# Kernel tuning notes

Hardware: AMD Instinct MI355X
Metric: run time of the kernel (lower is better)

## Reference

```python
import jax, jax.numpy as jnp
import numpy as np

DT = 0.05
DELAY = int(1.0 / DT)  # 20 steps of synaptic delay
NUM_ASCS = 2
R_MEM = 0.1     # membrane resistance
SIGMA_V = 1.0   # sigmoid smoothing of spiking nonlinearity
V_RESET = 0.0

B, T, IN, HID, OUT = 64, 200, 512, 1024, 512


def setup_inputs() -> dict:
    key = jax.random.key(0)
    ks = jax.random.split(key, 10)
    return {
        "x": jax.random.normal(ks[0], (B, T, IN), dtype=jnp.float32),
        "W_in": jax.random.normal(ks[1], (IN, HID), dtype=jnp.float32) / np.sqrt(IN),
        "W_lat": jax.random.normal(ks[2], (HID, HID), dtype=jnp.float32) / np.sqrt(HID),
        "thresh": jax.random.normal(ks[3], (1, HID), dtype=jnp.float32) * 0.1,
        "trans_k_m": jax.random.normal(ks[4], (1, HID), dtype=jnp.float32) * 0.1,
        "trans_asc_k": jax.random.normal(ks[5], (NUM_ASCS, 1, HID), dtype=jnp.float32) * 0.1,
        "asc_amp": jax.random.normal(ks[6], (NUM_ASCS, 1, HID), dtype=jnp.float32) * 0.1,
        "trans_asc_r": jax.random.normal(ks[7], (NUM_ASCS, 1, HID), dtype=jnp.float32) * 0.1,
        "W_out": jax.random.normal(ks[8], (OUT, HID), dtype=jnp.float32) / np.sqrt(HID),
        "b_out": jax.random.normal(ks[9], (OUT,), dtype=jnp.float32) * 0.01,
    }


def _glifr_rnn(x, W_in, W_lat, thresh, trans_k_m, trans_asc_k, asc_amp, trans_asc_r, W_out, b_out):
    Bx, Tx, _ = x.shape
    H = W_lat.shape[0]
    # rate transforms keep dt*k in (0,1); r in (-1,1)
    k_m = jax.nn.sigmoid(trans_k_m) / DT          # [1,H]
    k_asc = jax.nn.sigmoid(trans_asc_k) / DT      # [A,1,H]
    asc_r = 1.0 - 2.0 * jax.nn.sigmoid(trans_asc_r)
    # precompute input projection for all timesteps: [T,B,H]
    x_proj = jnp.swapaxes(jnp.einsum("bti,ih->bth", x, W_in), 0, 1)

    def step(carry, xp):
        firing, voltage, asc, buf = carry
        firing_delayed = buf[0]                       # firing DELAY steps ago
        syn = xp + firing_delayed @ W_lat             # synaptic current [B,H]
        asc_new = (asc_amp + asc_r * asc) * firing * (DT * k_asc) + (1.0 - DT * k_asc) * asc
        volt_new = (R_MEM * DT * k_m) * (syn + asc_new.sum(0)) \
                   + (1.0 - DT * k_m) * voltage + DT * k_m * V_RESET
        firing_new = jax.nn.sigmoid((volt_new - thresh) / SIGMA_V)
        buf_new = jnp.concatenate([buf[1:], firing_new[None]], axis=0)
        out = firing_new @ W_out.T + b_out            # per-step linear readout
        return (firing_new, volt_new, asc_new, buf_new), out

    z = jnp.zeros((Bx, H), dtype=x.dtype)
    carry0 = (z, z, jnp.zeros((NUM_ASCS, Bx, H), x.dtype), jnp.zeros((DELAY, Bx, H), x.dtype))
    _, outs = jax.lax.scan(step, carry0, x_proj)      # outs: [T,B,OUT]
    return jnp.swapaxes(outs, 0, 1)                   # [B,T,OUT]


def reference(x, W_in, W_lat, thresh, trans_k_m, trans_asc_k, asc_amp, trans_asc_r, W_out, b_out):
    return _glifr_rnn(x, W_in, W_lat, thresh, trans_k_m, trans_asc_k, asc_amp, trans_asc_r, W_out, b_out)
```

## Files before the change

### kernel.cpp

```cpp
#include <hip/hip_runtime.h>


typedef float f32x4 __attribute__((ext_vector_type(4)));
typedef __bf16 bf16x8 __attribute__((ext_vector_type(8)));
typedef unsigned short ushortx8 __attribute__((ext_vector_type(8)));
typedef unsigned short ushortx4 __attribute__((ext_vector_type(4)));

__device__ __forceinline__ unsigned short f2b(float f) {
    unsigned int u = __float_as_uint(f);
    unsigned int r = u + 0x7FFFu + ((u >> 16) & 1u);
    return (unsigned short)(r >> 16);
}
__device__ __forceinline__ float sigmoidf(float x) {
    return 1.0f / (1.0f + __expf(-x));
}

__device__ __forceinline__ void gl_lds16(const unsigned short* g, unsigned short* l) {
    __builtin_amdgcn_global_load_lds(
        (const __attribute__((address_space(1))) void*)g,
        (__attribute__((address_space(3))) void*)l, 16, 0, 0);
}

__global__ __launch_bounds__(256) void transpose_f32_to_bf16(
    const float* __restrict__ in, unsigned short* __restrict__ out,
    int R, int C)
{
    __shared__ unsigned short t[64][65];
    int bx = blockIdx.x * 64, by = blockIdx.y * 64;
    int tx = threadIdx.x & 63, ty = threadIdx.x >> 6;
    for (int r = ty; r < 64; r += 4)
        t[r][tx] = f2b(in[(size_t)(by + r) * C + bx + tx]);
    __syncthreads();
    for (int r = ty; r < 64; r += 4)
        out[(size_t)(bx + r) * R + by + tx] = t[tx][r];
}

__global__ __launch_bounds__(256) void convert_f32_to_bf16(
    const float* __restrict__ in, unsigned short* __restrict__ out)
{
    int i = (blockIdx.x * 256 + threadIdx.x) * 4;
    f32x4 v = *(const f32x4*)(in + i);
    ushortx4 o;
    o[0] = f2b(v[0]); o[1] = f2b(v[1]); o[2] = f2b(v[2]); o[3] = f2b(v[3]);
    *(ushortx4*)(out + i) = o;
}

__global__ __launch_bounds__(256) void convert_x(
    const float* __restrict__ x, unsigned short* __restrict__ xb)
{
    size_t i8 = (size_t)(blockIdx.x * 256 + threadIdx.x) * 8;
    int m = (int)(i8 >> 9), k = (int)(i8 & 511);
    int b = m & 63, t = m >> 6;
    const float* src = x + ((size_t)b * 200 + t) * 512 + k;
    f32x4 v0 = *(const f32x4*)src;
    f32x4 v1 = *(const f32x4*)(src + 4);
    ushortx8 o;
    o[0] = f2b(v0[0]); o[1] = f2b(v0[1]); o[2] = f2b(v0[2]); o[3] = f2b(v0[3]);
    o[4] = f2b(v1[0]); o[5] = f2b(v1[1]); o[6] = f2b(v1[2]); o[7] = f2b(v1[3]);
    *(ushortx8*)(xb + i8) = o;
}

template<int BM, int BN, int MODE>
__global__ __launch_bounds__(256) void gemm_nt(
    const unsigned short* __restrict__ A,
    const unsigned short* __restrict__ Bt,
    float* __restrict__ outf,
    const float* __restrict__ bias,
    int M, int N, int K, int t_base)
{
    constexpr int WM = BM / 2, WN = BN / 2;
    constexpr int TM = WM / 16, TN = WN / 16;

    __shared__ unsigned short Asm[BM * 64];
    __shared__ unsigned short Bsm[BN * 64];

    const int tid  = threadIdx.x;
    const int wave = tid >> 6, lane = tid & 63;
    const int m16  = lane & 15, quad = lane >> 4;
    const int bm0  = blockIdx.y * BM, bn0 = blockIdx.x * BN;
    const int wr   = (wave >> 1) * WM, wc = (wave & 1) * WN;
    const int sr   = lane >> 3;
    const int sc   = lane & 7;

    f32x4 acc[TM][TN];
#pragma unroll
    for (int i = 0; i < TM; i++)
#pragma unroll
        for (int j = 0; j < TN; j++)
            acc[i][j] = (f32x4){0.f, 0.f, 0.f, 0.f};

    for (int k0 = 0; k0 < K; k0 += 64) {
#pragma unroll
        for (int g = wave; g < BM / 8; g += 4) {
            int r = g * 8 + sr;
            int c = sc ^ (r & 7);
            gl_lds16(A + (size_t)(bm0 + r) * K + k0 + c * 8, Asm + g * 512);
        }
#pragma unroll
        for (int g = wave; g < BN / 8; g += 4) {
            int r = g * 8 + sr;
            int c = sc ^ (r & 7);
            gl_lds16(Bt + (size_t)(bn0 + r) * K + k0 + c * 8, Bsm + g * 512);
        }
        __syncthreads();

        ushortx8 af[2][TM], bfr[2][TN];
#pragma unroll
        for (int kh = 0; kh < 2; kh++) {
#pragma unroll
            for (int i = 0; i < TM; i++) {
                int ra = wr + i * 16 + m16;
                af[kh][i] = *(const ushortx8*)(
                    Asm + ra * 64 + (((kh * 4 + quad) ^ (ra & 7)) * 8));
            }
#pragma unroll
            for (int j = 0; j < TN; j++) {
                int rb = wc + j * 16 + m16;
                bfr[kh][j] = *(const ushortx8*)(
                    Bsm + rb * 64 + (((kh * 4 + quad) ^ (rb & 7)) * 8));
            }
        }
#pragma unroll
        for (int i = 0; i < TM; i++)
#pragma unroll
            for (int j = 0; j < TN; j++) {
                acc[i][j] = __builtin_amdgcn_mfma_f32_16x16x32_bf16(
                    __builtin_bit_cast(bf16x8, af[0][i]),
                    __builtin_bit_cast(bf16x8, bfr[0][j]),
                    acc[i][j], 0, 0, 0);
                acc[i][j] = __builtin_amdgcn_mfma_f32_16x16x32_bf16(
                    __builtin_bit_cast(bf16x8, af[1][i]),
                    __builtin_bit_cast(bf16x8, bfr[1][j]),
                    acc[i][j], 0, 0, 0);
            }
        __syncthreads();
    }

#pragma unroll
    for (int i = 0; i < TM; i++)
#pragma unroll
        for (int j = 0; j < TN; j++) {
            int col = bn0 + wc + j * 16 + m16;
            float bv = (MODE == 2) ? bias[col] : 0.f;
#pragma unroll
            for (int v = 0; v < 4; v++) {
                int row = bm0 + wr + i * 16 + quad * 4 + v;
                if (MODE == 2) {
                    size_t o = (size_t)((row & 63) * 200 + t_base + (row >> 6)) * N + col;
                    outf[o] = acc[i][j][v] + bv;
                } else {
                    outf[(size_t)row * N + col] = acc[i][j][v];
                }
            }
        }
}

__global__ __launch_bounds__(256) void fused_chunk(
    const unsigned short* __restrict__ Fprev,
    const unsigned short* __restrict__ Wlat,
    const float* __restrict__ xproj,
    float* __restrict__ state,
    unsigned short* __restrict__ Fc,
    const float* __restrict__ thresh,
    const float* __restrict__ t_km,
    const float* __restrict__ t_ak,
    const float* __restrict__ amp,
    const float* __restrict__ t_ar)
{
    const int BH = 64 * 1024;
    __shared__ __align__(16) char lds[36864];
    unsigned short* Asm = (unsigned short*)lds;
    unsigned short* Bsm = (unsigned short*)(lds + 20480);
    float* synT = (float*)lds;

    const int tid  = threadIdx.x;
    const int wave = tid >> 6, lane = tid & 63;
    const int m16  = lane & 15, quad = lane >> 4;
    const int sr4  = lane >> 4;
    const int sc16 = lane & 15;
    const int b0   = blockIdx.y * 4, h0 = blockIdx.x * 64;
    const int wrow = (wave >> 1) * 48;
    const int wc   = (wave & 1) * 32;

    f32x4 acc[3][2];
#pragma unroll
    for (int i = 0; i < 3; i++) {
        if (i < 2 || wave < 2) {
#pragma unroll
            for (int j = 0; j < 2; j++)
#pragma unroll
                for (int v = 0; v < 4; v++) {
                    int row = wrow + i * 16 + quad * 4 + v;
                    int col = h0 + wc + j * 16 + m16;
                    acc[i][j][v] = xproj[(size_t)(((row >> 2) << 6) + b0 + (row & 3)) * 1024 + col];
                }
        }
    }

    for (int k0 = 0; k0 < 1024; k0 += 128) {
        for (int g = wave; g < 20; g += 4) {
            int r = g * 4 + sr4;
            int c = sc16 ^ (r & 15);
            int m = ((r >> 2) << 6) + b0 + (r & 3);
            gl_lds16(Fprev + (size_t)m * 1024 + k0 + c * 8, Asm + g * 512);
        }
        for (int g = wave; g < 16; g += 4) {
            int r = g * 4 + sr4;
            int c = sc16 ^ (r & 15);
            gl_lds16(Wlat + (size_t)(h0 + r) * 1024 + k0 + c * 8, Bsm + g * 512);
        }
        __syncthreads();

        ushortx8 af[4][3], bfr[4][2];
#pragma unroll
        for (int kh = 0; kh < 4; kh++) {
#pragma unroll
            for (int i = 0; i < 3; i++) {
                if (i < 2 || wave < 2) {
                    int ra = wrow + i * 16 + m16;
                    af[kh][i] = *(const ushortx8*)(
                        Asm + ra * 128 + (((kh * 4 + quad) ^ (ra & 15)) * 8));
                }
            }
#pragma unroll
            for (int j = 0; j < 2; j++) {
                int rb = wc + j * 16 + m16;
                bfr[kh][j] = *(const ushortx8*)(
                    Bsm + rb * 128 + (((kh * 4 + quad) ^ (rb & 15)) * 8));
            }
        }
#pragma unroll
        for (int i = 0; i < 3; i++) {
            if (i < 2 || wave < 2) {
#pragma unroll
                for (int j = 0; j < 2; j++) {
#pragma unroll
                    for (int kh = 0; kh < 4; kh++) {
                        acc[i][j] = __builtin_amdgcn_mfma_f32_16x16x32_bf16(
                            __builtin_bit_cast(bf16x8, af[kh][i]),
                            __builtin_bit_cast(bf16x8, bfr[kh][j]), acc[i][j], 0, 0, 0);
                    }
                }
            }
        }
        __syncthreads();
    }

#pragma unroll
    for (int i = 0; i < 3; i++) {
        if (i < 2 || wave < 2) {
#pragma unroll
            for (int j = 0; j < 2; j++)
#pragma unroll
                for (int v = 0; v < 4; v++) {
                    int row = wrow + i * 16 + quad * 4 + v;
                    synT[row * 66 + wc + j * 16 + m16] = acc[i][j][v];
                }
        }
    }
    __syncthreads();

    const int h    = h0 + lane;
    const int gidx = (b0 + wave) * 1024 + h;
    float th  = thresh[h];
    float sm  = sigmoidf(t_km[h]);
    float rm  = 0.1f * sm;
    float om  = 1.0f - sm;
    float sa0 = sigmoidf(t_ak[h]);
    float sa1 = sigmoidf(t_ak[1024 + h]);
    float am0 = amp[h];
    float am1 = amp[1024 + h];
    float r0  = 1.0f - 2.0f * sigmoidf(t_ar[h]);
    float r1  = 1.0f - 2.0f * sigmoidf(t_ar[1024 + h]);

    float volt = state[gidx];
    float a0   = state[BH + gidx];
    float a1   = state[2 * BH + gidx];
    float fir  = state[3 * BH + gidx];

#pragma unroll
    for (int s = 0; s < 20; s++) {
        float sv  = synT[(s * 4 + wave) * 66 + lane];
        float na0 = (am0 + r0 * a0) * fir * sa0 + (1.f - sa0) * a0;
        float na1 = (am1 + r1 * a1) * fir * sa1 + (1.f - sa1) * a1;
        volt = rm * (sv + na0 + na1) + om * volt;
        fir  = sigmoidf(volt - th);
        Fc[(size_t)s * BH + gidx] = f2b(fir);
        a0 = na0; a1 = na1;
    }
    state[gidx]          = volt;
    state[BH + gidx]     = a0;
    state[2 * BH + gidx] = a1;
    state[3 * BH + gidx] = fir;
}

__global__ __launch_bounds__(256) void chunk_step(
    const float* __restrict__ syn,
    float* __restrict__ state,
    unsigned short* __restrict__ F,
    const float* __restrict__ thresh,
    const float* __restrict__ t_km,
    const float* __restrict__ t_ak,
    const float* __restrict__ amp,
    const float* __restrict__ t_ar)
{
    const int BH = 64 * 1024;
    int idx = blockIdx.x * 256 + threadIdx.x;
    int h = idx & 1023;

    float th  = thresh[h];
    float sm  = sigmoidf(t_km[h]);
    float rm  = 0.1f * sm;
    float om  = 1.0f - sm;
    float sa0 = sigmoidf(t_ak[h]);
    float sa1 = sigmoidf(t_ak[1024 + h]);
    float am0 = amp[h];
    float am1 = amp[1024 + h];
    float r0  = 1.0f - 2.0f * sigmoidf(t_ar[h]);
    float r1  = 1.0f - 2.0f * sigmoidf(t_ar[1024 + h]);

    float volt = 0.f, a0 = 0.f, a1 = 0.f, fir = 0.f;

#pragma unroll
    for (int s = 0; s < 20; s++) {
        float sv  = syn[(size_t)s * BH + idx];
        float na0 = (am0 + r0 * a0) * fir * sa0 + (1.f - sa0) * a0;
        float na1 = (am1 + r1 * a1) * fir * sa1 + (1.f - sa1) * a1;
        volt = rm * (sv + na0 + na1) + om * volt;
        fir  = sigmoidf(volt - th);
        F[(size_t)s * BH + idx] = f2b(fir);
        a0 = na0; a1 = na1;
    }
    state[idx]          = volt;
    state[BH + idx]     = a0;
    state[2 * BH + idx] = a1;
    state[3 * BH + idx] = fir;
}

extern "C" void kernel_launch(void* const* d_in, const int* in_sizes, int n_in,
                              void* d_out, int out_size, void* d_ws, size_t ws_size,
                              hipStream_t stream)
{
    const float* x      = (const float*)d_in[0];
    const float* W_in   = (const float*)d_in[1];
    const float* W_lat  = (const float*)d_in[2];
    const float* thresh = (const float*)d_in[3];
    const float* t_km   = (const float*)d_in[4];
    const float* t_ak   = (const float*)d_in[5];
    const float* amp    = (const float*)d_in[6];
    const float* t_ar   = (const float*)d_in[7];
    const float* W_out  = (const float*)d_in[8];
    const float* b_out  = (const float*)d_in[9];
    float* out = (float*)d_out;

    char* ws = (char*)d_ws;
    float*          syn   = (float*)ws;
    float*          state = (float*)(ws + 52428800);
    unsigned short* F     = (unsigned short*)(ws + 53477376);
    unsigned short* xb    = F;
    unsigned short* WinT  = (unsigned short*)(ws + 79691776);
    unsigned short* WlatT = (unsigned short*)(ws + 80740352);
    unsigned short* WoutB = (unsigned short*)(ws + 82837504);

    transpose_f32_to_bf16<<<dim3(16, 8),  256, 0, stream>>>(W_in,  WinT,  512,  1024);
    transpose_f32_to_bf16<<<dim3(16, 16), 256, 0, stream>>>(W_lat, WlatT, 1024, 1024);
    convert_f32_to_bf16<<<512, 256, 0, stream>>>(W_out, WoutB);
    convert_x<<<3200, 256, 0, stream>>>(x, xb);

    gemm_nt<128, 128, 0><<<dim3(1024 / 128, 12800 / 128), 256, 0, stream>>>(
        xb, WinT, syn, nullptr, 12800, 1024, 512, 0);

    chunk_step<<<256, 256, 0, stream>>>(syn, state, F, thresh, t_km, t_ak, amp, t_ar);

    const size_t CHUNK = 20 * 64 * 1024;
    for (int c = 1; c < 10; c++) {
        fused_chunk<<<dim3(16, 16), 256, 0, stream>>>(
            F + (size_t)(c - 1) * CHUNK, WlatT,
            syn + (size_t)c * CHUNK, state, F + (size_t)c * CHUNK,
            thresh, t_km, t_ak, amp, t_ar);
    }

    gemm_nt<128, 128, 2><<<dim3(512 / 128, 12800 / 128), 256, 0, stream>>>(
        F, WoutB, out, b_out, 12800, 512, 1024, 0);
}
```

Measured before the change: 280.5 us.

## Merge prep kernels into one launch and widen fused_chunk K tile to 512

Replaces the four separate weight/input conversion kernels with a single prep_all kernel that dispatches on block index, removing three kernel launches. In fused_chunk, the K loop now stages 512-wide slices of Fprev and W_lat into a 144 KB LDS buffer with a 64-way XOR swizzle, so each block makes two passes with two barriers instead of eight. The larger LDS footprint limits occupancy to one block per CU and front-loads more global traffic before compute starts, with no overlap of loads and MFMA.

```diff
diff --git a/kernel.cpp b/kernel.cpp
--- a/kernel.cpp
+++ b/kernel.cpp
@@ -21,43 +21,50 @@
         (__attribute__((address_space(3))) void*)l, 16, 0, 0);
 }
 
-__global__ __launch_bounds__(256) void transpose_f32_to_bf16(
-    const float* __restrict__ in, unsigned short* __restrict__ out,
-    int R, int C)
+__global__ __launch_bounds__(256) void prep_all(
+    const float* __restrict__ W_in, const float* __restrict__ W_lat,
+    const float* __restrict__ W_out, const float* __restrict__ x,
+    unsigned short* __restrict__ WinT, unsigned short* __restrict__ WlatT,
+    unsigned short* __restrict__ WoutB, unsigned short* __restrict__ xb)
 {
     __shared__ unsigned short t[64][65];
-    int bx = blockIdx.x * 64, by = blockIdx.y * 64;
-    int tx = threadIdx.x & 63, ty = threadIdx.x >> 6;
-    for (int r = ty; r < 64; r += 4)
-        t[r][tx] = f2b(in[(size_t)(by + r) * C + bx + tx]);
-    __syncthreads();
-    for (int r = ty; r < 64; r += 4)
-        out[(size_t)(bx + r) * R + by + tx] = t[tx][r];
-}
-
-__global__ __launch_bounds__(256) void convert_f32_to_bf16(
-    const float* __restrict__ in, unsigned short* __restrict__ out)
-{
-    int i = (blockIdx.x * 256 + threadIdx.x) * 4;
-    f32x4 v = *(const f32x4*)(in + i);
-    ushortx4 o;
-    o[0] = f2b(v[0]); o[1] = f2b(v[1]); o[2] = f2b(v[2]); o[3] = f2b(v[3]);
-    *(ushortx4*)(out + i) = o;
-}
-
-__global__ __launch_bounds__(256) void convert_x(
-    const float* __restrict__ x, unsigned short* __restrict__ xb)
-{
-    size_t i8 = (size_t)(blockIdx.x * 256 + threadIdx.x) * 8;
-    int m = (int)(i8 >> 9), k = (int)(i8 & 511);
-    int b = m & 63, t = m >> 6;
-    const float* src = x + ((size_t)b * 200 + t) * 512 + k;
-    f32x4 v0 = *(const f32x4*)src;
-    f32x4 v1 = *(const f32x4*)(src + 4);
-    ushortx8 o;
-    o[0] = f2b(v0[0]); o[1] = f2b(v0[1]); o[2] = f2b(v0[2]); o[3] = f2b(v0[3]);
-    o[4] = f2b(v1[0]); o[5] = f2b(v1[1]); o[6] = f2b(v1[2]); o[7] = f2b(v1[3]);
-    *(ushortx8*)(xb + i8) = o;
+    const int blk = blockIdx.x, tid = threadIdx.x;
+
+    if (blk < 128) {
+        int bx = (blk & 15) * 64, by = (blk >> 4) * 64;
+        int tx = tid & 63, ty = tid >> 6;
+        for (int r = ty; r < 64; r += 4)
+            t[r][tx] = f2b(W_in[(size_t)(by + r) * 1024 + bx + tx]);
+        __syncthreads();
+        for (int r = ty; r < 64; r += 4)
+            WinT[(size_t)(bx + r) * 512 + by + tx] = t[tx][r];
+    } else if (blk < 384) {
+        int b2 = blk - 128;
+        int bx = (b2 & 15) * 64, by = (b2 >> 4) * 64;
+        int tx = tid & 63, ty = tid >> 6;
+        for (int r = ty; r < 64; r += 4)
+            t[r][tx] = f2b(W_lat[(size_t)(by + r) * 1024 + bx + tx]);
+        __syncthreads();
+        for (int r = ty; r < 64; r += 4)
+            WlatT[(size_t)(bx + r) * 1024 + by + tx] = t[tx][r];
+    } else if (blk < 896) {
+        int i = ((blk - 384) * 256 + tid) * 4;
+        f32x4 v = *(const f32x4*)(W_out + i);
+        ushortx4 o;
+        o[0] = f2b(v[0]); o[1] = f2b(v[1]); o[2] = f2b(v[2]); o[3] = f2b(v[3]);
+        *(ushortx4*)(WoutB + i) = o;
+    } else {
+        size_t i8 = (size_t)((blk - 896) * 256 + tid) * 8;
+        int m = (int)(i8 >> 9), k = (int)(i8 & 511);
+        int b = m & 63, tt = m >> 6;
+        const float* src = x + ((size_t)b * 200 + tt) * 512 + k;
+        f32x4 v0 = *(const f32x4*)src;
+        f32x4 v1 = *(const f32x4*)(src + 4);
+        ushortx8 o;
+        o[0] = f2b(v0[0]); o[1] = f2b(v0[1]); o[2] = f2b(v0[2]); o[3] = f2b(v0[3]);
+        o[4] = f2b(v1[0]); o[5] = f2b(v1[1]); o[6] = f2b(v1[2]); o[7] = f2b(v1[3]);
+        *(ushortx8*)(xb + i8) = o;
+    }
 }
 
 template<int BM, int BN, int MODE>
@@ -168,16 +175,14 @@
     const float* __restrict__ t_ar)
 {
     const int BH = 64 * 1024;
-    __shared__ __align__(16) char lds[36864];
+    __shared__ __align__(16) char lds[147456];
     unsigned short* Asm = (unsigned short*)lds;
-    unsigned short* Bsm = (unsigned short*)(lds + 20480);
+    unsigned short* Bsm = (unsigned short*)(lds + 81920);
     float* synT = (float*)lds;
 
     const int tid  = threadIdx.x;
     const int wave = tid >> 6, lane = tid & 63;
     const int m16  = lane & 15, quad = lane >> 4;
-    const int sr4  = lane >> 4;
-    const int sc16 = lane & 15;
     const int b0   = blockIdx.y * 4, h0 = blockIdx.x * 64;
     const int wrow = (wave >> 1) * 48;
     const int wc   = (wave & 1) * 32;
@@ -197,48 +202,50 @@
         }
     }
 
-    for (int k0 = 0; k0 < 1024; k0 += 128) {
-        for (int g = wave; g < 20; g += 4) {
-            int r = g * 4 + sr4;
-            int c = sc16 ^ (r & 15);
-            int m = ((r >> 2) << 6) + b0 + (r & 3);
+    for (int k0 = 0; k0 < 1024; k0 += 512) {
+        for (int g = wave; g < 80; g += 4) {
+            int c = lane ^ (g & 63);
+            int m = ((g >> 2) << 6) + b0 + (g & 3);
             gl_lds16(Fprev + (size_t)m * 1024 + k0 + c * 8, Asm + g * 512);
         }
-        for (int g = wave; g < 16; g += 4) {
-            int r = g * 4 + sr4;
-            int c = sc16 ^ (r & 15);
-            gl_lds16(Wlat + (size_t)(h0 + r) * 1024 + k0 + c * 8, Bsm + g * 512);
-        }
-        __syncthreads();
-
-        ushortx8 af[4][3], bfr[4][2];
-#pragma unroll
-        for (int kh = 0; kh < 4; kh++) {
+        for (int g = wave; g < 64; g += 4) {
+            int c = lane ^ (g & 63);
+            gl_lds16(Wlat + (size_t)(h0 + g) * 1024 + k0 + c * 8, Bsm + g * 512);
+        }
+        __syncthreads();
+
+#pragma unroll
+        for (int qt = 0; qt < 4; qt++) {
+            ushortx8 af[4][3], bfr[4][2];
+#pragma unroll
+            for (int kh = 0; kh < 4; kh++) {
+                int s = qt * 16 + kh * 4 + quad;
+#pragma unroll
+                for (int i = 0; i < 3; i++) {
+                    if (i < 2 || wave < 2) {
+                        int ra = wrow + i * 16 + m16;
+                        af[kh][i] = *(const ushortx8*)(
+                            Asm + ra * 512 + ((s ^ (ra & 63)) * 8));
+                    }
+                }
+#pragma unroll
+                for (int j = 0; j < 2; j++) {
+                    int rb = wc + j * 16 + m16;
+                    bfr[kh][j] = *(const ushortx8*)(
+                        Bsm + rb * 512 + ((s ^ (rb & 63)) * 8));
+                }
+            }
 #pragma unroll
             for (int i = 0; i < 3; i++) {
                 if (i < 2 || wave < 2) {
-                    int ra = wrow + i * 16 + m16;
-                    af[kh][i] = *(const ushortx8*)(
-                        Asm + ra * 128 + (((kh * 4 + quad) ^ (ra & 15)) * 8));
-                }
-            }
-#pragma unroll
-            for (int j = 0; j < 2; j++) {
-                int rb = wc + j * 16 + m16;
-                bfr[kh][j] = *(const ushortx8*)(
-                    Bsm + rb * 128 + (((kh * 4 + quad) ^ (rb & 15)) * 8));
-            }
-        }
-#pragma unroll
-        for (int i = 0; i < 3; i++) {
-            if (i < 2 || wave < 2) {
-#pragma unroll
-                for (int j = 0; j < 2; j++) {
-#pragma unroll
-                    for (int kh = 0; kh < 4; kh++) {
-                        acc[i][j] = __builtin_amdgcn_mfma_f32_16x16x32_bf16(
-                            __builtin_bit_cast(bf16x8, af[kh][i]),
-                            __builtin_bit_cast(bf16x8, bfr[kh][j]), acc[i][j], 0, 0, 0);
+#pragma unroll
+                    for (int j = 0; j < 2; j++) {
+#pragma unroll
+                        for (int kh = 0; kh < 4; kh++) {
+                            acc[i][j] = __builtin_amdgcn_mfma_f32_16x16x32_bf16(
+                                __builtin_bit_cast(bf16x8, af[kh][i]),
+                                __builtin_bit_cast(bf16x8, bfr[kh][j]), acc[i][j], 0, 0, 0);
+                        }
                     }
                 }
             }
@@ -362,10 +369,8 @@
     unsigned short* WlatT = (unsigned short*)(ws + 80740352);
     unsigned short* WoutB = (unsigned short*)(ws + 82837504);
 
-    transpose_f32_to_bf16<<<dim3(16, 8),  256, 0, stream>>>(W_in,  WinT,  512,  1024);
-    transpose_f32_to_bf16<<<dim3(16, 16), 256, 0, stream>>>(W_lat, WlatT, 1024, 1024);
-    convert_f32_to_bf16<<<512, 256, 0, stream>>>(W_out, WoutB);
-    convert_x<<<3200, 256, 0, stream>>>(x, xb);
+    prep_all<<<4096, 256, 0, stream>>>(W_in, W_lat, W_out, x,
+                                       WinT, WlatT, WoutB, xb);
 
     gemm_nt<128, 128, 0><<<dim3(1024 / 128, 12800 / 128), 256, 0, stream>>>(
         xb, WinT, syn, nullptr, 12800, 1024, 512, 0);
```

Measured after the change: 256.4 us. 1.09x faster.
